# Kernel tuning notes

Measured on AMD Instinct MI355X. Metric: run time of the kernel, lower is better.

Reference implementation:

```python
import jax, jax.numpy as jnp
import numpy as np

N_ADAPTERS = 8
RANK = 64  # per-adapter LoRA rank (uniform here; ragged in general)
SCALINGS = np.full((N_ADAPTERS,), 2.0, dtype=np.float32)  # alpha / r


def setup_inputs() -> dict:
    key = jax.random.key(0)
    k1, k2, k3, k4, k5 = jax.random.split(key, 5)
    T, DIN, DOUT = 8192, 4096, 4096
    total_rank = N_ADAPTERS * RANK
    x = jax.random.normal(k1, (T, DIN), dtype=jnp.float32)
    lora_A = jax.random.normal(k2, (total_rank, DIN), dtype=jnp.float32) * 0.02
    lora_B = jax.random.normal(k3, (total_rank, DOUT), dtype=jnp.float32) * 0.02
    base_output = jax.random.normal(k4, (T, DOUT), dtype=jnp.float32)
    adapter_ids = jax.random.randint(k5, (T,), 0, N_ADAPTERS, dtype=jnp.int64)
    return {"x": x, "lora_A": lora_A, "lora_B": lora_B,
            "base_output": base_output, "adapter_ids": adapter_ids}


def reference(x, lora_A, lora_B, base_output, adapter_ids):
    """Multi-adapter LoRA: out = base + scaling[a] * (x @ A_a.T) @ B_a per token.

    base_slice covers the full out_features here, so the LoRA delta is added
    to the whole base_output. Loop is over the small fixed adapter set.
    """
    lora_out = jnp.zeros_like(base_output)
    for a in range(N_ADAPTERS):
        A_a = lora_A[a * RANK:(a + 1) * RANK]  # [R, DIN]
        B_a = lora_B[a * RANK:(a + 1) * RANK]  # [R, DOUT]
        xa = x @ A_a.T                          # [T, R]
        mask = (adapter_ids == a).astype(x.dtype)[:, None]
        lora_out = lora_out + SCALINGS[a] * ((xa * mask) @ B_a)
    return base_output + lora_out
```

## Files before the change

kernel.cpp:

```cpp
#include <hip/hip_runtime.h>
#include <hip/hip_bf16.h>

#define T_TOK 8192
#define DIN   4096
#define DOUT  4096
#define RANK  64
#define NAD   8
#define TS    32
#define MAXTILES 264
#define TOTR  (NAD*RANK)
#define KSPLIT 4
#define KCH   (DIN / KSPLIT)
#define NT    (KCH / 64)
#define DSPLIT 8
#define DCH   (DOUT / DSPLIT)
#define NS    (DCH / 64)

typedef __bf16 bf16x8 __attribute__((ext_vector_type(8)));
typedef __bf16 bf16x4 __attribute__((ext_vector_type(4)));
typedef float  f32x4  __attribute__((ext_vector_type(4)));

#define WS_CURSORS 0
#define WS_NTILES  64
#define WS_FLAG    128
#define WS_TINFO   256
#define WS_PERM    4096
#define WS_XA      0x10000
#define WS_ABF     0x110000
#define WS_BT      0x510000
#define WS_XAP     0x910000
#define WS_END     (0x910000 + (size_t)KSPLIT * T_TOK * RANK * 4)

__device__ __forceinline__ void gll16(const void* g, void* l) {
  __builtin_amdgcn_global_load_lds(
      (const __attribute__((address_space(1))) unsigned int*)g,
      (__attribute__((address_space(3))) unsigned int*)l, 16, 0, 0);
}

__global__ __launch_bounds__(1024) void hist_prep(const int* __restrict__ ids,
    int* __restrict__ cursors, int* __restrict__ ntilesp,
    int* __restrict__ flagp, int* __restrict__ tinfo) {
  __shared__ int cnt[NAD];
  __shared__ int s_ofs[NAD], s_tbase[NAD + 1];
  __shared__ int s_is64;
  int tid = threadIdx.x, lane = tid & 63;
  if (tid < NAD) cnt[tid] = 0;
  if (tid == 0) s_is64 = 1;
  __syncthreads();
  int any = 0;
  for (int i = tid; i < T_TOK; i += 1024)
    if (i & 1) any |= ids[i];
  if (any) s_is64 = 0;
  __syncthreads();
  int is64 = s_is64;
  int loc[NAD];
#pragma unroll
  for (int a = 0; a < NAD; ++a) loc[a] = 0;
  for (int t = tid; t < T_TOK; t += 1024) {
    int id = (is64 ? ids[2 * t] : ids[t]) & 7;
#pragma unroll
    for (int a = 0; a < NAD; ++a) {
      unsigned long long m = __ballot(id == a);
      if (lane == 0) loc[a] += __popcll(m);
    }
  }
  if (lane == 0) {
#pragma unroll
    for (int a = 0; a < NAD; ++a) if (loc[a]) atomicAdd(&cnt[a], loc[a]);
  }
  __syncthreads();
  if (tid == 0) {
    *flagp = is64;
    int ofs = 0, tb = 0;
    for (int a = 0; a < NAD; ++a) {
      s_ofs[a] = ofs; cursors[a] = ofs;
      s_tbase[a] = tb;
      ofs += cnt[a];
      tb += (cnt[a] + TS - 1) / TS;
    }
    s_tbase[NAD] = tb;
    *ntilesp = tb;
  }
  __syncthreads();
  int ntt = s_tbase[NAD];
  for (int e = tid; e < ntt; e += 1024) {
    int a = 0;
    while (e >= s_tbase[a + 1]) ++a;
    int t0 = (e - s_tbase[a]) * TS;
    int c = cnt[a];
    tinfo[e * 3 + 0] = a;
    tinfo[e * 3 + 1] = s_ofs[a] + t0;
    tinfo[e * 3 + 2] = (c - t0 < TS) ? (c - t0) : TS;
  }
}

__global__ __launch_bounds__(256) void scatter_k(const int* __restrict__ ids,
    const int* __restrict__ flagp, int* __restrict__ cursors, int* __restrict__ perm) {
  int t = blockIdx.x * 256 + threadIdx.x;
  int lane = threadIdx.x & 63;
  int id = ((*flagp) ? ids[2 * t] : ids[t]) & 7;
  unsigned long long lt = (1ull << lane) - 1ull;
#pragma unroll
  for (int a = 0; a < NAD; ++a) {
    unsigned long long m = __ballot(id == a);
    if (m) {
      int leader = __ffsll((long long)m) - 1;
      int base_a = 0;
      if (lane == leader) base_a = atomicAdd(&cursors[a], __popcll(m));
      base_a = __shfl(base_a, leader, 64);
      if (id == a) perm[base_a + __popcll(m & lt)] = t;
    }
  }
}

__global__ __launch_bounds__(256) void conv_a(const float* __restrict__ A,
                                              __bf16* __restrict__ Abf) {
  int i = blockIdx.x * 256 + threadIdx.x;
  float4 v = ((const float4*)A)[i];
  bf16x4 o = { (__bf16)v.x, (__bf16)v.y, (__bf16)v.z, (__bf16)v.w };
  ((bf16x4*)Abf)[i] = o;
}

__global__ __launch_bounds__(256) void trans_b(const float* __restrict__ B,
                                               __bf16* __restrict__ Bt) {
  __shared__ float t[64][65];
  int rb = blockIdx.x, db = blockIdx.y;
  int tid = threadIdx.x;
  int c = tid & 63, q = tid >> 6;
#pragma unroll
  for (int i = 0; i < 16; ++i) {
    int r = i * 4 + q;
    t[r][c] = B[(size_t)(rb * 64 + r) * DOUT + db * 64 + c];
  }
  __syncthreads();
#pragma unroll
  for (int i = 0; i < 16; ++i) {
    int d = i * 4 + q;
    Bt[(size_t)(db * 64 + d) * TOTR + rb * 64 + c] = (__bf16)t[c][d];
  }
}

#define CVT8(lo, hi) { (__bf16)lo.x, (__bf16)lo.y, (__bf16)lo.z, (__bf16)lo.w, \
                       (__bf16)hi.x, (__bf16)hi.y, (__bf16)hi.z, (__bf16)hi.w }

__global__ __launch_bounds__(512) void stage1s(const float* __restrict__ x,
    const __bf16* __restrict__ Abf, const int* __restrict__ tinfo,
    const int* __restrict__ ntilesp, const int* __restrict__ perm,
    float* __restrict__ xap) {
  __shared__ char lds[2][16384];
  int b = blockIdx.x;
  if (b >= *ntilesp) return;
  int ks = blockIdx.y;
  int a = tinfo[b * 3], start = tinfo[b * 3 + 1], nv = tinfo[b * 3 + 2];
  int tid = threadIdx.x, lane = tid & 63, wv = tid >> 6;

  int xr = wv * 4 + (lane >> 4);
  int xtok = (xr < nv) ? perm[start + xr] : perm[start];
  int xinner = ((lane & 15) * 16) ^ ((xr & 7) << 4);
  const char* xsrc = (const char*)(x + (size_t)xtok * DIN + ks * KCH) + xinner;
  int ar = wv * 8 + (lane >> 3);
  int ainner = ((lane & 7) * 16) ^ ((ar & 7) << 4);
  const char* asrc = (const char*)(Abf + (size_t)(a * RANK + ar) * DIN + ks * KCH) + ainner;

  int l16 = lane & 15, lq = lane >> 4;
  int rb = wv & 1, cb = wv >> 1;
  int xrow = rb * 16 + l16;
  int arow = cb * 16 + l16;
  int swx = (xrow & 7) << 4;
  int swa = (arow & 7) << 4;

  f32x4 acc = {0.f, 0.f, 0.f, 0.f};

  gll16(xsrc, &lds[0][wv * 1024]);
  gll16(asrc, &lds[0][8192 + wv * 1024]);

  for (int t = 0; t < NT; ++t) {
    const char* cbuf = lds[t & 1];
    if (t + 1 < NT) {
      char* nbuf = lds[(t + 1) & 1];
      gll16(xsrc + (size_t)(t + 1) * 256, nbuf + wv * 1024);
      gll16(asrc + (size_t)(t + 1) * 128, nbuf + 8192 + wv * 1024);
      asm volatile("s_waitcnt vmcnt(2)" ::: "memory");
    } else {
      asm volatile("s_waitcnt vmcnt(0)" ::: "memory");
    }
    __builtin_amdgcn_s_barrier();
    asm volatile("" ::: "memory");
#pragma unroll
    for (int m = 0; m < 2; ++m) {
      f32x4 xv0 = *(const f32x4*)(cbuf + xrow * 256 + ((m * 128 + lq * 32) ^ swx));
      f32x4 xv1 = *(const f32x4*)(cbuf + xrow * 256 + ((m * 128 + lq * 32 + 16) ^ swx));
      bf16x8 xf = { (__bf16)xv0[0], (__bf16)xv0[1], (__bf16)xv0[2], (__bf16)xv0[3],
                    (__bf16)xv1[0], (__bf16)xv1[1], (__bf16)xv1[2], (__bf16)xv1[3] };
      bf16x8 af = *(const bf16x8*)(cbuf + 8192 + arow * 128 + ((m * 64 + lq * 16) ^ swa));
      acc = __builtin_amdgcn_mfma_f32_16x16x32_bf16(xf, af, acc, 0, 0, 0);
    }
    asm volatile("" ::: "memory");
    __builtin_amdgcn_s_barrier();
  }

  float* xo = xap + (size_t)ks * T_TOK * RANK;
#pragma unroll
  for (int j = 0; j < 4; ++j) {
    int tr = rb * 16 + lq * 4 + j;
    if (tr < nv) {
      int tk = perm[start + tr];
      xo[(size_t)tk * RANK + cb * 16 + l16] = acc[j];
    }
  }
}

__global__ __launch_bounds__(256) void reduce_xa(const float* __restrict__ xap,
                                                 __bf16* __restrict__ xa) {
  int i = blockIdx.x * 256 + threadIdx.x;
  const float4* p = (const float4*)xap;
  float4 s = p[i];
#pragma unroll
  for (int ks = 1; ks < KSPLIT; ++ks) {
    float4 q = p[(size_t)ks * (T_TOK * RANK / 4) + i];
    s.x += q.x; s.y += q.y; s.z += q.z; s.w += q.w;
  }
  bf16x4 o = { (__bf16)s.x, (__bf16)s.y, (__bf16)s.z, (__bf16)s.w };
  ((bf16x4*)xa)[i] = o;
}

__global__ __launch_bounds__(512) void stage1f(const float* __restrict__ x,
    const __bf16* __restrict__ Abf, const int* __restrict__ tinfo,
    const int* __restrict__ ntilesp, const int* __restrict__ perm,
    __bf16* __restrict__ xa) {
  int b = blockIdx.x;
  if (b >= *ntilesp) return;
  int a = tinfo[b * 3], start = tinfo[b * 3 + 1], nv = tinfo[b * 3 + 2];
  int tid = threadIdx.x, lane = tid & 63, w = tid >> 6;
  int rb = w & 1, cb = w >> 1;
  int l16 = lane & 15, lq = lane >> 4;
  int trow = rb * 16 + l16;
  int tok = (trow < nv) ? perm[start + trow] : 0;
  const float*  xrow = x + (size_t)tok * DIN + lq * 8;
  const __bf16* arow = Abf + (size_t)(a * RANK + cb * 16 + l16) * DIN + lq * 8;
  f32x4 acc = {0.f, 0.f, 0.f, 0.f};
#pragma unroll 4
  for (int k0 = 0; k0 < DIN; k0 += 32) {
    float4 v0 = *(const float4*)(xrow + k0);
    float4 v1 = *(const float4*)(xrow + k0 + 4);
    bf16x8 af = CVT8(v0, v1);
    bf16x8 bfr = *(const bf16x8*)(arow + k0);
    acc = __builtin_amdgcn_mfma_f32_16x16x32_bf16(af, bfr, acc, 0, 0, 0);
  }
#pragma unroll
  for (int j = 0; j < 4; ++j) {
    int tr = rb * 16 + lq * 4 + j;
    if (tr < nv) {
      int tk = perm[start + tr];
      xa[(size_t)tk * RANK + cb * 16 + l16] = (__bf16)acc[j];
    }
  }
}

__global__ __launch_bounds__(512) void stage2(const __bf16* __restrict__ xa,
    const __bf16* __restrict__ Bt, const float* __restrict__ base,
    const int* __restrict__ tinfo, const int* __restrict__ ntilesp,
    const int* __restrict__ perm, float* __restrict__ out) {
  __shared__ char lds[2][16384];
  int b = blockIdx.y;
  if (b >= *ntilesp) return;
  int a = tinfo[b * 3], start = tinfo[b * 3 + 1], nv = tinfo[b * 3 + 2];
  int tid = threadIdx.x, lane = tid & 63, wv = tid >> 6;
  int dblk = blockIdx.x * DCH;

  int brow = wv * 4 + (lane >> 4);
  int btok = (brow < nv) ? perm[start + brow] : perm[start];
  int binner = ((lane & 15) * 16) ^ ((brow & 7) << 4);
  const char* bsrc = (const char*)(base + (size_t)btok * DOUT + dblk) + binner;
  int trow = wv * 8 + (lane >> 3);
  int tinner = ((lane & 7) * 16) ^ ((trow & 7) << 4);
  const char* tsrc = (const char*)(Bt + (size_t)(dblk + trow) * TOTR + a * RANK) + tinner;

  int tb = wv & 1, dg = wv >> 1;
  int l16 = lane & 15, lq = lane >> 4;
  int tIdx = tb * 16 + l16;
  bool valid = tIdx < nv;
  int token = valid ? perm[start + tIdx] : perm[start];

  const __bf16* xrow = xa + (size_t)token * RANK + lq * 8;
  bf16x8 xv0 = *(const bf16x8*)(xrow);
  bf16x8 xv1 = *(const bf16x8*)(xrow + 32);

  float* orow = out + (size_t)token * DOUT + dblk + dg * 16 + lq * 4;

  int btrow = dg * 16 + l16;
  int btoff0 = btrow * 128 + ((lq * 16) ^ ((btrow & 7) << 4));
  int btoff1 = btrow * 128 + ((lq * 16 + 64) ^ ((btrow & 7) << 4));
  int bsoff  = tIdx * 256 + ((dg * 64 + lq * 16) ^ ((tIdx & 7) << 4));

  f32x4 res[NS];

  asm volatile("" ::: "memory");
  gll16(bsrc, &lds[0][wv * 1024]);
  gll16(tsrc, &lds[0][8192 + wv * 1024]);

#pragma unroll
  for (int t = 0; t < NS; ++t) {
    const char* cbuf = lds[t & 1];
    if (t + 1 < NS) {
      char* nbuf = lds[(t + 1) & 1];
      gll16(bsrc + (size_t)(t + 1) * 256,   nbuf + wv * 1024);
      gll16(tsrc + (size_t)(t + 1) * 65536, nbuf + 8192 + wv * 1024);
      asm volatile("s_waitcnt vmcnt(2)" ::: "memory");
    } else {
      asm volatile("s_waitcnt vmcnt(0)" ::: "memory");
    }
    __builtin_amdgcn_s_barrier();
    asm volatile("" ::: "memory");
    bf16x8 bf0 = *(const bf16x8*)(cbuf + 8192 + btoff0);
    bf16x8 bf1 = *(const bf16x8*)(cbuf + 8192 + btoff1);
    f32x4  bs  = *(const f32x4*)(cbuf + bsoff);
    f32x4 z = {0.f, 0.f, 0.f, 0.f};
    z = __builtin_amdgcn_mfma_f32_16x16x32_bf16(bf0, xv0, z, 0, 0, 0);
    z = __builtin_amdgcn_mfma_f32_16x16x32_bf16(bf1, xv1, z, 0, 0, 0);
    res[t][0] = bs[0] + 2.0f * z[0];
    res[t][1] = bs[1] + 2.0f * z[1];
    res[t][2] = bs[2] + 2.0f * z[2];
    res[t][3] = bs[3] + 2.0f * z[3];
    asm volatile("" ::: "memory");
    __builtin_amdgcn_s_barrier();
  }

  if (valid) {
#pragma unroll
    for (int t = 0; t < NS; ++t)
      *(float4*)(orow + t * 64) = *(const float4*)&res[t];
  }
}

extern "C" void kernel_launch(void* const* d_in, const int* in_sizes, int n_in,
                              void* d_out, int out_size, void* d_ws, size_t ws_size,
                              hipStream_t stream) {
  const float* x   = (const float*)d_in[0];
  const float* A   = (const float*)d_in[1];
  const float* B   = (const float*)d_in[2];
  const float* bas = (const float*)d_in[3];
  const int*   ids = (const int*)d_in[4];
  float* out = (float*)d_out;
  char* ws = (char*)d_ws;
  int* cursors = (int*)(ws + WS_CURSORS);
  int* ntiles  = (int*)(ws + WS_NTILES);
  int* flag    = (int*)(ws + WS_FLAG);
  int* tinfo   = (int*)(ws + WS_TINFO);
  int* perm    = (int*)(ws + WS_PERM);
  __bf16* xa   = (__bf16*)(ws + WS_XA);
  __bf16* Abf  = (__bf16*)(ws + WS_ABF);
  __bf16* Bt   = (__bf16*)(ws + WS_BT);
  float*  xap  = (float*)(ws + WS_XAP);

  hist_prep<<<1, 1024, 0, stream>>>(ids, cursors, ntiles, flag, tinfo);
  scatter_k<<<T_TOK / 256, 256, 0, stream>>>(ids, flag, cursors, perm);
  conv_a<<<(TOTR * DIN / 4) / 256, 256, 0, stream>>>(A, Abf);
  trans_b<<<dim3(TOTR / 64, DOUT / 64), 256, 0, stream>>>(B, Bt);
  if (ws_size >= WS_END) {
    stage1s<<<dim3(MAXTILES, KSPLIT), 512, 0, stream>>>(x, Abf, tinfo, ntiles, perm, xap);
    reduce_xa<<<(T_TOK * RANK / 4) / 256, 256, 0, stream>>>(xap, xa);
  } else {
    stage1f<<<MAXTILES, 512, 0, stream>>>(x, Abf, tinfo, ntiles, perm, xa);
  }
  stage2<<<dim3(DSPLIT, MAXTILES), 512, 0, stream>>>(xa, Bt, bas, tinfo, ntiles, perm, out);
}
```

Measured before the change: 146.3 us.

## Deepen LDS prefetch to four buffers and merge A/B prep kernels

Both GEMM stages move from a two-buffer LDS ring to a four-buffer ring with three loads in flight. The trailing per-iteration barrier is removed by issuing the next prefetch only after the leading barrier, into a slot that no wave can still be reading. The A conversion and B transpose kernels are merged into one launch to save a kernel launch and let the two run concurrently. LDS use doubles to 64KB per block, which may reduce occupancy.

```diff
diff --git a/kernel.cpp b/kernel.cpp
--- a/kernel.cpp
+++ b/kernel.cpp
@@ -113,30 +113,30 @@
   }
 }
 
-__global__ __launch_bounds__(256) void conv_a(const float* __restrict__ A,
-                                              __bf16* __restrict__ Abf) {
-  int i = blockIdx.x * 256 + threadIdx.x;
-  float4 v = ((const float4*)A)[i];
-  bf16x4 o = { (__bf16)v.x, (__bf16)v.y, (__bf16)v.z, (__bf16)v.w };
-  ((bf16x4*)Abf)[i] = o;
-}
-
-__global__ __launch_bounds__(256) void trans_b(const float* __restrict__ B,
-                                               __bf16* __restrict__ Bt) {
-  __shared__ float t[64][65];
-  int rb = blockIdx.x, db = blockIdx.y;
-  int tid = threadIdx.x;
-  int c = tid & 63, q = tid >> 6;
-#pragma unroll
-  for (int i = 0; i < 16; ++i) {
-    int r = i * 4 + q;
-    t[r][c] = B[(size_t)(rb * 64 + r) * DOUT + db * 64 + c];
-  }
-  __syncthreads();
-#pragma unroll
-  for (int i = 0; i < 16; ++i) {
-    int d = i * 4 + q;
-    Bt[(size_t)(db * 64 + d) * TOTR + rb * 64 + c] = (__bf16)t[c][d];
+__global__ __launch_bounds__(256) void prep_ab(const float* __restrict__ A,
+    __bf16* __restrict__ Abf, const float* __restrict__ B, __bf16* __restrict__ Bt) {
+  if (blockIdx.x < 2048) {
+    int i = blockIdx.x * 256 + threadIdx.x;
+    float4 v = ((const float4*)A)[i];
+    bf16x4 o = { (__bf16)v.x, (__bf16)v.y, (__bf16)v.z, (__bf16)v.w };
+    ((bf16x4*)Abf)[i] = o;
+  } else {
+    __shared__ float t[64][65];
+    int idx = blockIdx.x - 2048;
+    int rb = idx & 7, db = idx >> 3;
+    int tid = threadIdx.x;
+    int c = tid & 63, q = tid >> 6;
+#pragma unroll
+    for (int i = 0; i < 16; ++i) {
+      int r = i * 4 + q;
+      t[r][c] = B[(size_t)(rb * 64 + r) * DOUT + db * 64 + c];
+    }
+    __syncthreads();
+#pragma unroll
+    for (int i = 0; i < 16; ++i) {
+      int d = i * 4 + q;
+      Bt[(size_t)(db * 64 + d) * TOTR + rb * 64 + c] = (__bf16)t[c][d];
+    }
   }
 }
 
@@ -147,7 +147,7 @@
     const __bf16* __restrict__ Abf, const int* __restrict__ tinfo,
     const int* __restrict__ ntilesp, const int* __restrict__ perm,
     float* __restrict__ xap) {
-  __shared__ char lds[2][16384];
+  __shared__ char lds[4][16384];
   int b = blockIdx.x;
   if (b >= *ntilesp) return;
   int ks = blockIdx.y;
@@ -171,21 +171,24 @@
 
   f32x4 acc = {0.f, 0.f, 0.f, 0.f};
 
-  gll16(xsrc, &lds[0][wv * 1024]);
-  gll16(asrc, &lds[0][8192 + wv * 1024]);
+#pragma unroll
+  for (int p = 0; p < 3; ++p) {
+    gll16(xsrc + (size_t)p * 256, &lds[p][wv * 1024]);
+    gll16(asrc + (size_t)p * 128, &lds[p][8192 + wv * 1024]);
+  }
 
   for (int t = 0; t < NT; ++t) {
-    const char* cbuf = lds[t & 1];
-    if (t + 1 < NT) {
-      char* nbuf = lds[(t + 1) & 1];
-      gll16(xsrc + (size_t)(t + 1) * 256, nbuf + wv * 1024);
-      gll16(asrc + (size_t)(t + 1) * 128, nbuf + 8192 + wv * 1024);
-      asm volatile("s_waitcnt vmcnt(2)" ::: "memory");
-    } else {
-      asm volatile("s_waitcnt vmcnt(0)" ::: "memory");
-    }
+    if (t < NT - 2)       asm volatile("s_waitcnt vmcnt(4)" ::: "memory");
+    else if (t == NT - 2) asm volatile("s_waitcnt vmcnt(2)" ::: "memory");
+    else                  asm volatile("s_waitcnt vmcnt(0)" ::: "memory");
     __builtin_amdgcn_s_barrier();
     asm volatile("" ::: "memory");
+    if (t + 3 < NT) {
+      char* nbuf = lds[(t + 3) & 3];
+      gll16(xsrc + (size_t)(t + 3) * 256, nbuf + wv * 1024);
+      gll16(asrc + (size_t)(t + 3) * 128, nbuf + 8192 + wv * 1024);
+    }
+    const char* cbuf = lds[t & 3];
 #pragma unroll
     for (int m = 0; m < 2; ++m) {
       f32x4 xv0 = *(const f32x4*)(cbuf + xrow * 256 + ((m * 128 + lq * 32) ^ swx));
@@ -196,7 +199,6 @@
       acc = __builtin_amdgcn_mfma_f32_16x16x32_bf16(xf, af, acc, 0, 0, 0);
     }
     asm volatile("" ::: "memory");
-    __builtin_amdgcn_s_barrier();
   }
 
   float* xo = xap + (size_t)ks * T_TOK * RANK;
@@ -261,7 +263,7 @@
     const __bf16* __restrict__ Bt, const float* __restrict__ base,
     const int* __restrict__ tinfo, const int* __restrict__ ntilesp,
     const int* __restrict__ perm, float* __restrict__ out) {
-  __shared__ char lds[2][16384];
+  __shared__ char lds[4][16384];
   int b = blockIdx.y;
   if (b >= *ntilesp) return;
   int a = tinfo[b * 3], start = tinfo[b * 3 + 1], nv = tinfo[b * 3 + 2];
@@ -296,22 +298,25 @@
   f32x4 res[NS];
 
   asm volatile("" ::: "memory");
-  gll16(bsrc, &lds[0][wv * 1024]);
-  gll16(tsrc, &lds[0][8192 + wv * 1024]);
+#pragma unroll
+  for (int p = 0; p < 3; ++p) {
+    gll16(bsrc + (size_t)p * 256,   &lds[p][wv * 1024]);
+    gll16(tsrc + (size_t)p * 65536, &lds[p][8192 + wv * 1024]);
+  }
 
 #pragma unroll
   for (int t = 0; t < NS; ++t) {
-    const char* cbuf = lds[t & 1];
-    if (t + 1 < NS) {
-      char* nbuf = lds[(t + 1) & 1];
-      gll16(bsrc + (size_t)(t + 1) * 256,   nbuf + wv * 1024);
-      gll16(tsrc + (size_t)(t + 1) * 65536, nbuf + 8192 + wv * 1024);
-      asm volatile("s_waitcnt vmcnt(2)" ::: "memory");
-    } else {
-      asm volatile("s_waitcnt vmcnt(0)" ::: "memory");
-    }
+    if (t < NS - 2)       asm volatile("s_waitcnt vmcnt(4)" ::: "memory");
+    else if (t == NS - 2) asm volatile("s_waitcnt vmcnt(2)" ::: "memory");
+    else                  asm volatile("s_waitcnt vmcnt(0)" ::: "memory");
     __builtin_amdgcn_s_barrier();
     asm volatile("" ::: "memory");
+    if (t + 3 < NS) {
+      char* nbuf = lds[(t + 3) & 3];
+      gll16(bsrc + (size_t)(t + 3) * 256,   nbuf + wv * 1024);
+      gll16(tsrc + (size_t)(t + 3) * 65536, nbuf + 8192 + wv * 1024);
+    }
+    const char* cbuf = lds[t & 3];
     bf16x8 bf0 = *(const bf16x8*)(cbuf + 8192 + btoff0);
     bf16x8 bf1 = *(const bf16x8*)(cbuf + 8192 + btoff1);
     f32x4  bs  = *(const f32x4*)(cbuf + bsoff);
@@ -323,7 +328,6 @@
     res[t][2] = bs[2] + 2.0f * z[2];
     res[t][3] = bs[3] + 2.0f * z[3];
     asm volatile("" ::: "memory");
-    __builtin_amdgcn_s_barrier();
   }
 
   if (valid) {
@@ -355,8 +359,7 @@
 
   hist_prep<<<1, 1024, 0, stream>>>(ids, cursors, ntiles, flag, tinfo);
   scatter_k<<<T_TOK / 256, 256, 0, stream>>>(ids, flag, cursors, perm);
-  conv_a<<<(TOTR * DIN / 4) / 256, 256, 0, stream>>>(A, Abf);
-  trans_b<<<dim3(TOTR / 64, DOUT / 64), 256, 0, stream>>>(B, Bt);
+  prep_ab<<<2048 + 512, 256, 0, stream>>>(A, Abf, B, Bt);
   if (ws_size >= WS_END) {
     stage1s<<<dim3(MAXTILES, KSPLIT), 512, 0, stream>>>(x, Abf, tinfo, ntiles, perm, xap);
     reduce_xa<<<(T_TOK * RANK / 4) / 256, 256, 0, stream>>>(xap, xa);
```

Measured after the change: 149.1 us. About the same (+1.9%).
